# Kernel optimization log

Hardware: AMD Instinct MI355X
Metric: run time of the kernel (lower is better)

## Reference

```python
import jax, jax.numpy as jnp
import numpy as np

SHADOW_OFFSET = -1000.0
EPS_SIGMA = 1e-05
SIGMA_DIV = 2.1


def setup_inputs() -> dict:
    key = jax.random.key(0)
    k1, k2, k3, k4, k5, k6 = jax.random.split(key, 6)
    B, N, M, K, Kp, Din, Dout = 2, 65536, 16384, 32, 15, 64, 128
    points_xyz = jax.random.normal(k1, (B, N, 3), dtype=jnp.float32)
    features = jax.random.normal(k2, (B, Din, N), dtype=jnp.float32)
    center_xyz = jax.random.normal(k3, (B, M, 3), dtype=jnp.float32)
    neighbor_indices = jax.random.randint(k4, (B, M, K), 0, N + 1, dtype=jnp.int64)
    # kernel points in unit ball, 'center' fixed at origin (stand-in for load_kernels)
    kp = jax.random.normal(k5, (Kp, 3), dtype=jnp.float32)
    kp = kp / (jnp.linalg.norm(kp, axis=-1, keepdims=True) + 1e-6) * jax.random.uniform(k6, (Kp, 1)) ** (1.0 / 3.0)
    kernel_points = kp.at[0].set(0.0)
    # kaiming_uniform(a=sqrt(5)) on [Kp, Din, Dout]: fan_in = Din*Dout per torch semantics
    fan_in = Din * Dout
    bound = jnp.sqrt(6.0 / ((1.0 + 5.0) * fan_in)) * jnp.sqrt(3.0) / jnp.sqrt(3.0)
    bound = float(np.sqrt(6.0 / (6.0 * fan_in)))
    weights = jax.random.uniform(jax.random.fold_in(key, 7), (Kp, Din, Dout), minval=-bound, maxval=bound, dtype=jnp.float32)
    return {"points_xyz": points_xyz, "features": features, "center_xyz": center_xyz,
            "neighbor_indices": neighbor_indices, "kernel_points": kernel_points, "weights": weights}


def reference(points_xyz, features, center_xyz, neighbor_indices, kernel_points, weights):
    B, N, _ = points_xyz.shape
    M, K = neighbor_indices.shape[1], neighbor_indices.shape[2]
    Din = features.shape[1]
    # [B,N,3+Din] point coords + features, plus shadow point at index N
    points = jnp.concatenate([points_xyz, jnp.swapaxes(features, 1, 2)], axis=-1)
    shadow = jnp.zeros((B, 1, 3 + Din), points.dtype).at[:, :, :3].set(SHADOW_OFFSET)
    points = jnp.concatenate([points, shadow], axis=1)  # [B,N+1,3+Din]
    idx = neighbor_indices.reshape(B, M * K)
    gathered = jnp.take_along_axis(points, idx[:, :, None], axis=1).reshape(B, M, K, 3 + Din)
    neighbors_xyz = gathered[..., :3] - center_xyz[:, :, None, :]   # [B,M,K,3]
    neighbors_feats = gathered[..., 3:]                              # [B,M,K,Din]
    dist = jnp.sqrt(jnp.sum(neighbors_xyz ** 2, axis=3))             # [B,M,K]
    m_dist = jnp.max(dist, axis=2, keepdims=True)                    # [B,M,1]
    # radius=None path: kernel points scaled per center by max neighbor distance
    kp = kernel_points[None, None, :, :] * m_dist[:, :, :, None]     # [B,M,Kp,3]
    diffs = neighbors_xyz[:, :, :, None, :] - kp[:, :, None, :, :]   # [B,M,K,Kp,3]
    sq_d = jnp.sum(diffs ** 2, axis=4)                               # [B,M,K,Kp]
    sigma = m_dist[..., None] / SIGMA_DIV + EPS_SIGMA                # [B,M,1,1]
    w = jnp.clip(1.0 - jnp.sqrt(sq_d) / sigma, 0.0)                  # [B,M,K,Kp]
    weighted = jnp.einsum('bmkp,bmkd->bmpd', w, neighbors_feats)     # [B,M,Kp,Din]
    out = jnp.einsum('bmpd,pdo->bmo', weighted, weights)             # [B,M,Dout]
    return jnp.swapaxes(out, 1, 2)                                   # [B,Dout,M]
```

## Files before the change

kernel.cpp:

```cpp
#include <hip/hip_runtime.h>
#include <hip/hip_bf16.h>
#include <stdint.h>

#define B_    2
#define N_    65536
#define M_    16384
#define K_    32
#define KP_   15
#define DIN_  64
#define DOUT_ 128

typedef __bf16 bf16x8 __attribute__((ext_vector_type(8)));
typedef float  f32x4  __attribute__((ext_vector_type(4)));

__device__ inline float bf2f(unsigned int u) {
    union { unsigned int i; float f; } v; v.i = u << 16; return v.f;
}
__device__ inline unsigned short f2bf(float f) {
    union { float f; unsigned int i; } v; v.f = f;
    unsigned int x = v.i;
    return (unsigned short)((x + 0x7fffu + ((x >> 16) & 1u)) >> 16);
}

__global__ __launch_bounds__(256) void transpose_feats(const float* __restrict__ feats,
                                                       unsigned short* __restrict__ featT) {
    const int b  = blockIdx.y;
    const int n0 = blockIdx.x * 64;
    const int t  = threadIdx.x;
    if (n0 >= N_) {
        if (t < 32)
            ((unsigned int*)(featT + ((size_t)b * (N_ + 1) + N_) * DIN_))[t] = 0u;
        return;
    }
    __shared__ float tile[64][65];
    const int nl = t & 63, dl = t >> 6;
    #pragma unroll
    for (int i = 0; i < 16; ++i) {
        int d = dl + 4 * i;
        tile[d][nl] = feats[((size_t)b * DIN_ + d) * N_ + n0 + nl];
    }
    __syncthreads();
    const int d2 = (t & 31) * 2;
    const int nr = t >> 5;
    #pragma unroll
    for (int i = 0; i < 8; ++i) {
        int n = nr + 8 * i;
        unsigned int u = ((unsigned int)f2bf(tile[d2 + 1][n]) << 16) | f2bf(tile[d2][n]);
        ((unsigned int*)(featT + ((size_t)b * (N_ + 1) + n0 + n) * DIN_))[t & 31] = u;
    }
}

__global__ __launch_bounds__(256) void build_wt(const float* __restrict__ w,
                                                unsigned short* __restrict__ wt) {
    int tid = blockIdx.x * 256 + threadIdx.x;
    if (tid < 960 * 128) {
        int pd = tid >> 7, o = tid & 127;
        wt[o * 960 + pd] = f2bf(w[tid]);
    }
}

__global__ __launch_bounds__(256, 3) void gather_weight(
    const float* __restrict__ points_xyz,
    const float* __restrict__ center_xyz,
    const int*   __restrict__ nidx,
    const float* __restrict__ kpts,
    const unsigned short* __restrict__ featT,
    unsigned short* __restrict__ weighted) {

    __shared__ __align__(16) float        wlds[8 * KP_ * 32];
    __shared__ __align__(16) unsigned int fbuf[8 * 32 * 32];

    const int t  = threadIdx.x;
    const int b  = blockIdx.y;
    const int m0 = blockIdx.x * 8;
    const size_t ibase = ((size_t)b * M_ + m0) * K_;

    uint4 v[8];
    const int part = t & 7, rbase = t >> 3;
    #pragma unroll
    for (int i = 0; i < 8; ++i) {
        int r = i * 32 + rbase;
        int n = nidx[ibase + r];
        v[i] = *(const uint4*)(featT + ((size_t)b * (N_ + 1) + n) * DIN_ + part * 8);
    }

    {
        const int m = t >> 5, k = t & 31;
        int n = nidx[ibase + t];
        float px, py, pz;
        if (n < N_) {
            const float* p = points_xyz + ((size_t)b * N_ + n) * 3;
            px = p[0]; py = p[1]; pz = p[2];
        } else {
            px = py = pz = -1000.0f;
        }
        const float* c = center_xyz + ((size_t)b * M_ + m0 + m) * 3;
        float dx = px - c[0], dy = py - c[1], dz = pz - c[2];
        float md = sqrtf(dx * dx + dy * dy + dz * dz);
        #pragma unroll
        for (int s = 16; s > 0; s >>= 1)
            md = fmaxf(md, __shfl_xor(md, s));
        float rsig = 1.0f / (md / 2.1f + 1e-5f);
        #pragma unroll
        for (int p = 0; p < KP_; ++p) {
            float ex = dx - kpts[p * 3 + 0] * md;
            float ey = dy - kpts[p * 3 + 1] * md;
            float ez = dz - kpts[p * 3 + 2] * md;
            float wv = 1.0f - sqrtf(ex * ex + ey * ey + ez * ez) * rsig;
            wlds[(m * KP_ + p) * 32 + k] = wv > 0.0f ? wv : 0.0f;
        }
    }

    #pragma unroll
    for (int i = 0; i < 8; ++i)
        ((uint4*)fbuf)[(i * 32 + rbase) * 8 + part] = v[i];
    __syncthreads();

    const int m = t >> 5, d2 = t & 31;
    float acc[KP_][2];
    #pragma unroll
    for (int p = 0; p < KP_; ++p) { acc[p][0] = 0.f; acc[p][1] = 0.f; }

    for (int k4 = 0; k4 < 8; ++k4) {
        float f0[4], f1[4];
        #pragma unroll
        for (int j = 0; j < 4; ++j) {
            unsigned int u = fbuf[(m * 32 + k4 * 4 + j) * 32 + d2];
            f0[j] = bf2f(u & 0xffffu); f1[j] = bf2f(u >> 16);
        }
        #pragma unroll
        for (int p = 0; p < KP_; ++p) {
            float4 w4 = *(const float4*)&wlds[(m * KP_ + p) * 32 + k4 * 4];
            acc[p][0] += w4.x * f0[0]; acc[p][0] += w4.y * f0[1];
            acc[p][0] += w4.z * f0[2]; acc[p][0] += w4.w * f0[3];
            acc[p][1] += w4.x * f1[0]; acc[p][1] += w4.y * f1[1];
            acc[p][1] += w4.z * f1[2]; acc[p][1] += w4.w * f1[3];
        }
    }

    unsigned int* wout = (unsigned int*)weighted + (size_t)(b * M_ + m0 + m) * 480 + d2;
    #pragma unroll
    for (int p = 0; p < KP_; ++p) {
        unsigned int u = ((unsigned int)f2bf(acc[p][1]) << 16) | f2bf(acc[p][0]);
        wout[p * 32] = u;
    }
}

#define GLOAD_LDS16(g, l) __builtin_amdgcn_global_load_lds( \
    (const __attribute__((address_space(1))) unsigned int*)(g), \
    (__attribute__((address_space(3))) unsigned int*)(l), 16, 0, 0)

__global__ __launch_bounds__(512, 2) void gemm_out(
    const unsigned short* __restrict__ weightedG,
    const unsigned short* __restrict__ wtG,
    float* __restrict__ out) {

    __shared__ __align__(16) char smem[65536];

    const int t = threadIdx.x;
    const int w = t >> 6, lane = t & 63;
    const int bm0 = blockIdx.x * 128;
    const int b = bm0 >> 14, m_in_b = bm0 & (M_ - 1);

    const int wr = w >> 2, wc = w & 3;
    const int wm = wr * 64, wo = wc * 32;

    f32x4 acc[4][2] = {};

    auto stage = [&](int buf, int kt) {
        #pragma unroll
        for (int i = 0; i < 2; ++i) {
            int chunk = w * 2 + i;
            int L = chunk * 1024 + lane * 16;
            int row = L >> 7, col = L & 127;
            int scol = col ^ ((row & 7) << 4);
            const char* src = (const char*)weightedG + (size_t)(bm0 + row) * 1920 + kt * 128 + scol;
            GLOAD_LDS16(src, smem + buf * 16384 + chunk * 1024);
        }
        #pragma unroll
        for (int i = 0; i < 2; ++i) {
            int chunk = w * 2 + i;
            int L = chunk * 1024 + lane * 16;
            int row = L >> 7, col = L & 127;
            int scol = col ^ ((row & 7) << 4);
            const char* src = (const char*)wtG + (size_t)row * 1920 + kt * 128 + scol;
            GLOAD_LDS16(src, smem + 32768 + buf * 16384 + chunk * 1024);
        }
    };

    stage(0, 0);
    __syncthreads();

    for (int kt = 0; kt < 15; ++kt) {
        int cur = kt & 1;
        if (kt < 14) stage(cur ^ 1, kt + 1);
        const char* lA = smem + cur * 16384;
        const char* lB = smem + 32768 + cur * 16384;
        #pragma unroll
        for (int ks = 0; ks < 2; ++ks) {
            bf16x8 af[4], bfr[2];
            const int kcol = ks * 64 + (lane >> 4) * 16;
            #pragma unroll
            for (int mf = 0; mf < 4; ++mf) {
                int row = wm + mf * 16 + (lane & 15);
                af[mf] = *(const bf16x8*)(lA + row * 128 + (kcol ^ ((row & 7) << 4)));
            }
            #pragma unroll
            for (int of = 0; of < 2; ++of) {
                int row = wo + of * 16 + (lane & 15);
                bfr[of] = *(const bf16x8*)(lB + row * 128 + (kcol ^ ((row & 7) << 4)));
            }
            #pragma unroll
            for (int mf = 0; mf < 4; ++mf)
                #pragma unroll
                for (int of = 0; of < 2; ++of)
                    acc[mf][of] = __builtin_amdgcn_mfma_f32_16x16x32_bf16(
                        af[mf], bfr[of], acc[mf][of], 0, 0, 0);
        }
        __syncthreads();
    }

    #pragma unroll
    for (int mf = 0; mf < 4; ++mf)
        #pragma unroll
        for (int of = 0; of < 2; ++of) {
            int o  = wo + of * 16 + (lane & 15);
            int mr = wm + mf * 16 + (lane >> 4) * 4;
            int byte = (o * 512 + mr * 4) ^ ((o & 7) << 4);
            *(f32x4*)(smem + byte) = acc[mf][of];
        }
    __syncthreads();
    #pragma unroll
    for (int pass = 0; pass < 4; ++pass) {
        int o  = pass * 32 + (t >> 4);
        int mc = (t & 15) * 8;
        int b0 = (o * 512 + mc * 4)       ^ ((o & 7) << 4);
        int b1 = (o * 512 + (mc + 4) * 4) ^ ((o & 7) << 4);
        f32x4 v0 = *(const f32x4*)(smem + b0);
        f32x4 v1 = *(const f32x4*)(smem + b1);
        float* dst = out + ((size_t)(b * DOUT_ + o)) * M_ + m_in_b + mc;
        *(f32x4*)dst = v0;
        *(f32x4*)(dst + 4) = v1;
    }
}

extern "C" void kernel_launch(void* const* d_in, const int* in_sizes, int n_in,
                              void* d_out, int out_size, void* d_ws, size_t ws_size,
                              hipStream_t stream) {
    const float* points_xyz = (const float*)d_in[0];
    const float* features   = (const float*)d_in[1];
    const float* center_xyz = (const float*)d_in[2];
    const int*   nidx       = (const int*)d_in[3];
    const float* kpts       = (const float*)d_in[4];
    const float* weights    = (const float*)d_in[5];
    float* out = (float*)d_out;

    unsigned short* featT    = (unsigned short*)d_ws;
    unsigned short* wt       = (unsigned short*)((char*)d_ws + 16777472);
    unsigned short* weighted = (unsigned short*)((char*)d_ws + 17023232);

    transpose_feats<<<dim3((N_ + 64) / 64, B_), 256, 0, stream>>>(features, featT);
    build_wt<<<480, 256, 0, stream>>>(weights, wt);
    gather_weight<<<dim3(M_ / 8, B_), 256, 0, stream>>>(points_xyz, center_xyz, nidx,
                                                        kpts, featT, weighted);
    gemm_out<<<B_ * M_ / 128, 512, 0, stream>>>(weighted, wt, out);
}
```

Before: 159.4 us.

## Compute KPConv kernel-point weighting with bf16 MFMA instead of scalar FMAs

Replaces the scalar per-thread accumulation of weights times neighbour features with a 16x16x32 bf16 MFMA per center and feature tile. Influence weights are computed in registers per lane and converted to bf16, and features are stored in an XOR-swizzled LDS buffer. This drops the fp32 weight LDS buffer and the heavy FMA loop, and raises occupancy from 3 to 4 blocks. The catch is that the influence weights are now rounded to bf16 and the neighbour coordinates are loaded by more lanes.

```diff
diff --git a/kernel.cpp b/kernel.cpp
--- a/kernel.cpp
+++ b/kernel.cpp
@@ -59,7 +59,7 @@
     }
 }
 
-__global__ __launch_bounds__(256, 3) void gather_weight(
+__global__ __launch_bounds__(256, 4) void gather_weight_mfma(
     const float* __restrict__ points_xyz,
     const float* __restrict__ center_xyz,
     const int*   __restrict__ nidx,
@@ -67,82 +67,90 @@
     const unsigned short* __restrict__ featT,
     unsigned short* __restrict__ weighted) {
 
-    __shared__ __align__(16) float        wlds[8 * KP_ * 32];
-    __shared__ __align__(16) unsigned int fbuf[8 * 32 * 32];
+    __shared__ __align__(16) char Fb[8 * 32 * 128];
 
     const int t  = threadIdx.x;
     const int b  = blockIdx.y;
     const int m0 = blockIdx.x * 8;
     const size_t ibase = ((size_t)b * M_ + m0) * K_;
 
+    const int part = t & 7, rbase = t >> 3;
+    const int kswz = (rbase & 24) << 2;
     uint4 v[8];
-    const int part = t & 7, rbase = t >> 3;
     #pragma unroll
     for (int i = 0; i < 8; ++i) {
-        int r = i * 32 + rbase;
-        int n = nidx[ibase + r];
+        int n = nidx[ibase + i * 32 + rbase];
         v[i] = *(const uint4*)(featT + ((size_t)b * (N_ + 1) + n) * DIN_ + part * 8);
     }
-
-    {
-        const int m = t >> 5, k = t & 31;
-        int n = nidx[ibase + t];
-        float px, py, pz;
-        if (n < N_) {
-            const float* p = points_xyz + ((size_t)b * N_ + n) * 3;
-            px = p[0]; py = p[1]; pz = p[2];
-        } else {
-            px = py = pz = -1000.0f;
-        }
-        const float* c = center_xyz + ((size_t)b * M_ + m0 + m) * 3;
-        float dx = px - c[0], dy = py - c[1], dz = pz - c[2];
-        float md = sqrtf(dx * dx + dy * dy + dz * dz);
-        #pragma unroll
-        for (int s = 16; s > 0; s >>= 1)
-            md = fmaxf(md, __shfl_xor(md, s));
-        float rsig = 1.0f / (md / 2.1f + 1e-5f);
-        #pragma unroll
-        for (int p = 0; p < KP_; ++p) {
-            float ex = dx - kpts[p * 3 + 0] * md;
-            float ey = dy - kpts[p * 3 + 1] * md;
-            float ez = dz - kpts[p * 3 + 2] * md;
+    #pragma unroll
+    for (int i = 0; i < 8; ++i) {
+        int byte = (((i * 32 + rbase) << 7) + part * 16) ^ kswz;
+        *(uint4*)(Fb + byte) = v[i];
+    }
+    __syncthreads();
+
+    const int w0 = t >> 6, l = t & 63;
+    const int p  = l & 15, ks = l >> 4;
+    const int kp_i = p < KP_ ? p : KP_ - 1;
+    const float kpx = kpts[kp_i * 3 + 0];
+    const float kpy = kpts[kp_i * 3 + 1];
+    const float kpz = kpts[kp_i * 3 + 2];
+    const int aswz = ks << 5;
+
+    #pragma unroll
+    for (int mi = 0; mi < 2; ++mi) {
+        const int m  = w0 * 2 + mi;
+        const int bm = b * M_ + m0 + m;
+        const float cx = center_xyz[bm * 3 + 0];
+        const float cy = center_xyz[bm * 3 + 1];
+        const float cz = center_xyz[bm * 3 + 2];
+
+        float dx[8], dy[8], dz[8];
+        float mymax = 0.f;
+        #pragma unroll
+        for (int j = 0; j < 8; ++j) {
+            int n = nidx[ibase + m * 32 + ks * 8 + j];
+            float px, py, pz;
+            if (n < N_) {
+                const float* pp = points_xyz + ((size_t)b * N_ + n) * 3;
+                px = pp[0]; py = pp[1]; pz = pp[2];
+            } else { px = py = pz = -1000.0f; }
+            dx[j] = px - cx; dy[j] = py - cy; dz[j] = pz - cz;
+            float dist = sqrtf(dx[j] * dx[j] + dy[j] * dy[j] + dz[j] * dz[j]);
+            mymax = fmaxf(mymax, dist);
+        }
+        mymax = fmaxf(mymax, __shfl_xor(mymax, 16));
+        mymax = fmaxf(mymax, __shfl_xor(mymax, 32));
+        const float md   = mymax;
+        const float rsig = 1.0f / (md * (1.0f / 2.1f) + 1e-5f);
+
+        union { unsigned short us[8]; bf16x8 v; } wf;
+        #pragma unroll
+        for (int j = 0; j < 8; ++j) {
+            float ex = dx[j] - kpx * md;
+            float ey = dy[j] - kpy * md;
+            float ez = dz[j] - kpz * md;
             float wv = 1.0f - sqrtf(ex * ex + ey * ey + ez * ez) * rsig;
-            wlds[(m * KP_ + p) * 32 + k] = wv > 0.0f ? wv : 0.0f;
-        }
-    }
-
-    #pragma unroll
-    for (int i = 0; i < 8; ++i)
-        ((uint4*)fbuf)[(i * 32 + rbase) * 8 + part] = v[i];
-    __syncthreads();
-
-    const int m = t >> 5, d2 = t & 31;
-    float acc[KP_][2];
-    #pragma unroll
-    for (int p = 0; p < KP_; ++p) { acc[p][0] = 0.f; acc[p][1] = 0.f; }
-
-    for (int k4 = 0; k4 < 8; ++k4) {
-        float f0[4], f1[4];
-        #pragma unroll
-        for (int j = 0; j < 4; ++j) {
-            unsigned int u = fbuf[(m * 32 + k4 * 4 + j) * 32 + d2];
-            f0[j] = bf2f(u & 0xffffu); f1[j] = bf2f(u >> 16);
-        }
-        #pragma unroll
-        for (int p = 0; p < KP_; ++p) {
-            float4 w4 = *(const float4*)&wlds[(m * KP_ + p) * 32 + k4 * 4];
-            acc[p][0] += w4.x * f0[0]; acc[p][0] += w4.y * f0[1];
-            acc[p][0] += w4.z * f0[2]; acc[p][0] += w4.w * f0[3];
-            acc[p][1] += w4.x * f1[0]; acc[p][1] += w4.y * f1[1];
-            acc[p][1] += w4.z * f1[2]; acc[p][1] += w4.w * f1[3];
-        }
-    }
-
-    unsigned int* wout = (unsigned int*)weighted + (size_t)(b * M_ + m0 + m) * 480 + d2;
-    #pragma unroll
-    for (int p = 0; p < KP_; ++p) {
-        unsigned int u = ((unsigned int)f2bf(acc[p][1]) << 16) | f2bf(acc[p][0]);
-        wout[p * 32] = u;
+            wf.us[j] = f2bf(wv > 0.f ? wv : 0.f);
+        }
+
+        #pragma unroll
+        for (int dt = 0; dt < 4; ++dt) {
+            union { unsigned short us[8]; bf16x8 v; } af;
+            #pragma unroll
+            for (int j = 0; j < 8; ++j) {
+                int byte = (((m * 32 + ks * 8 + j) << 7) + (dt * 16 + p) * 2) ^ aswz;
+                af.us[j] = *(const unsigned short*)(Fb + byte);
+            }
+            f32x4 d1 = __builtin_amdgcn_mfma_f32_16x16x32_bf16(
+                af.v, wf.v, (f32x4){0.f, 0.f, 0.f, 0.f}, 0, 0, 0);
+            if (p < KP_) {
+                uint2 u;
+                u.x = ((unsigned int)f2bf(d1[1]) << 16) | f2bf(d1[0]);
+                u.y = ((unsigned int)f2bf(d1[3]) << 16) | f2bf(d1[2]);
+                *(uint2*)(weighted + (size_t)bm * 960 + p * 64 + dt * 16 + ks * 4) = u;
+            }
+        }
     }
 }
 
@@ -261,7 +269,7 @@
 
     transpose_feats<<<dim3((N_ + 64) / 64, B_), 256, 0, stream>>>(features, featT);
     build_wt<<<480, 256, 0, stream>>>(weights, wt);
-    gather_weight<<<dim3(M_ / 8, B_), 256, 0, stream>>>(points_xyz, center_xyz, nidx,
-                                                        kpts, featT, weighted);
+    gather_weight_mfma<<<dim3(M_ / 8, B_), 256, 0, stream>>>(points_xyz, center_xyz, nidx,
+                                                             kpts, featT, weighted);
     gemm_out<<<B_ * M_ / 128, 512, 0, stream>>>(weighted, wt, out);
 }
```

Measured after the change: 174.6 us. +9.5%, slower.
